# Performance work log

Hardware: AMD Instinct MI355X
Metric: run time of the kernel (lower is better)

Reference implementation:

```python
import jax, jax.numpy as jnp
import numpy as np

B, S, D, H = 2, 2048, 1024, 16
DH = D // H
NEG = -1000000.0


def setup_inputs() -> dict:
    key = jax.random.key(0)
    k1, k2, k3, k4, k5, k6 = jax.random.split(key, 6)
    query = jax.random.normal(k1, (B, S, D), dtype=jnp.float32)
    key_t = jax.random.normal(k2, (B, S, D), dtype=jnp.float32)
    value = jax.random.normal(k3, (B, S, D), dtype=jnp.float32)
    # causal boolean mask, broadcast to [B*H, S, S] as the torch module expects
    causal = jnp.tril(jnp.ones((S, S), dtype=bool))
    attn_mask = jnp.broadcast_to(causal, (B * H, S, S))
    WQ = jax.random.normal(k4, (D, D), dtype=jnp.float32) * 0.02
    WK = jax.random.normal(k5, (D, D), dtype=jnp.float32) * 0.02
    WV = jax.random.normal(k6, (D, D), dtype=jnp.float32) * 0.02
    return {"query": query, "key": key_t, "value": value,
            "attn_mask": attn_mask, "WQ": WQ, "WK": WK, "WV": WV}


def reference(query, key, value, attn_mask, WQ, WK, WV):
    b, s, d = query.shape
    h = attn_mask.shape[0] // b
    dh = d // h
    # Linear projections (bias=False) then torch's split(dim=2)+concat(dim=0)
    # == reshape to [b,s,h,dh] and move head axis to the front: [h,b,s,dh]
    q = (query @ WQ).reshape(b, s, h, dh).transpose(2, 0, 1, 3)
    k = (key @ WK).reshape(b, s, h, dh).transpose(2, 0, 1, 3)
    v = (value @ WV).reshape(b, s, h, dh).transpose(2, 0, 1, 3)
    mask = attn_mask.reshape(h, b, s, s)
    add_mask = jnp.where(mask, jnp.float32(0.0), jnp.float32(NEG))
    # NOTE: original adds the mask BEFORE dividing by sqrt(dh) (baddbmm then /=)
    scores = (jnp.einsum('hbqd,hbkd->hbqk', q, k) + add_mask) / jnp.float32(dh ** 0.5)
    p = jax.nn.softmax(scores, axis=-1)
    p = p * mask.astype(p.dtype)  # mask applied a second time post-softmax
    out = jnp.einsum('hbqk,hbkd->hbqd', p, v)  # [h,b,s,dh]
    # concat heads back on the feature dim: [b,s,d]
    return out.transpose(1, 2, 0, 3).reshape(b, s, d)
```

## Files before the change

kernel.cpp:

```cpp
#include <hip/hip_runtime.h>
#include <hip/hip_bf16.h>

#define B_  2
#define S_  2048
#define D_  1024
#define H_  16
#define DH_ 64
#define BH_ (B_ * H_)
#define M_  (B_ * S_)

typedef __bf16 bf16x8 __attribute__((ext_vector_type(8)));
typedef __bf16 bf16x4 __attribute__((ext_vector_type(4)));
typedef float  f32x4  __attribute__((ext_vector_type(4)));

__device__ __forceinline__ __bf16 to_bf16(float f) {
  union { float f; unsigned u; } un; un.f = f;
  unsigned r = un.u + 0x7FFFu + ((un.u >> 16) & 1u);
  union { unsigned short s; __bf16 b; } o;
  o.s = (unsigned short)(r >> 16);
  return o.b;
}

__device__ __forceinline__ void async_load16(const __bf16* g, __bf16* l) {
  __builtin_amdgcn_global_load_lds(
      (const __attribute__((address_space(1))) void*)g,
      (__attribute__((address_space(3))) void*)l, 16, 0, 0);
}

__global__ __launch_bounds__(256) void convert_x_kernel(
    const float* __restrict__ q_in, const float* __restrict__ k_in,
    const float* __restrict__ v_in, __bf16* __restrict__ Xb) {
  const float* src = blockIdx.z == 0 ? q_in : (blockIdx.z == 1 ? k_in : v_in);
  __bf16* dst = Xb + (size_t)blockIdx.z * M_ * D_;
  const size_t i = ((size_t)blockIdx.x * 256 + threadIdx.x) * 4;
  const float4 f = *(const float4*)(src + i);
  bf16x4 o;
  o[0] = to_bf16(f.x); o[1] = to_bf16(f.y); o[2] = to_bf16(f.z); o[3] = to_bf16(f.w);
  *(bf16x4*)(dst + i) = o;
}

__global__ void transpose_w_kernel(const float* __restrict__ Wq,
                                   const float* __restrict__ Wk,
                                   const float* __restrict__ Wv,
                                   __bf16* __restrict__ WT) {
  __shared__ float tile[32][33];
  const float* src = blockIdx.z == 0 ? Wq : (blockIdx.z == 1 ? Wk : Wv);
  __bf16* dst = WT + (size_t)blockIdx.z * D_ * D_;
  const int tx = threadIdx.x, ty = threadIdx.y;
  const int j  = blockIdx.x * 32 + tx;
  const int k0 = blockIdx.y * 32;
#pragma unroll
  for (int i = 0; i < 32; i += 8)
    tile[ty + i][tx] = src[(size_t)(k0 + ty + i) * D_ + j];
  __syncthreads();
  const int jr = blockIdx.x * 32;
  const int kc = k0 + tx;
#pragma unroll
  for (int i = 0; i < 32; i += 8)
    dst[(size_t)(jr + ty + i) * D_ + kc] = to_bf16(tile[tx][ty + i]);
}

__global__ __launch_bounds__(256) void proj_kernel(
    const __bf16* __restrict__ Xb, const __bf16* __restrict__ WT,
    __bf16* __restrict__ Qo, __bf16* __restrict__ Ko, __bf16* __restrict__ VTo) {
  const int lane = threadIdx.x & 63;
  const int wave = threadIdx.x >> 6;
  const int lr   = lane & 15;
  const int quad = lane >> 4;
  const int wr   = wave >> 1;
  const int wc   = wave & 1;
  const int which = blockIdx.z;
  const __bf16* X  = Xb + (size_t)which * M_ * D_;
  const __bf16* Wt = WT + (size_t)which * D_ * D_;
  const int m0 = blockIdx.y * 128;
  const int n0 = blockIdx.x * 128;

  __shared__ __align__(16) __bf16 As[128 * 32];
  __shared__ __align__(16) __bf16 Bs[128 * 32];

  f32x4 acc[4][4];
#pragma unroll
  for (int a = 0; a < 4; ++a)
#pragma unroll
    for (int b = 0; b < 4; ++b)
      acc[a][b] = f32x4{0.f, 0.f, 0.f, 0.f};

  const int srow  = (lane >> 2);
  const int schnk = (lane & 3) * 8;

  for (int kt = 0; kt < D_ / 32; ++kt) {
    const int k0 = kt * 32;
#pragma unroll
    for (int r16 = 0; r16 < 2; ++r16) {
      const int row = wave * 32 + r16 * 16 + srow;
      async_load16(X  + (size_t)(m0 + row) * D_ + k0 + schnk,
                   As + (size_t)(wave * 32 + r16 * 16) * 32);
      async_load16(Wt + (size_t)(n0 + row) * D_ + k0 + schnk,
                   Bs + (size_t)(wave * 32 + r16 * 16) * 32);
    }
    __syncthreads();

    bf16x8 af[4], bf[4];
#pragma unroll
    for (int mi = 0; mi < 4; ++mi)
      af[mi] = *(const bf16x8*)(As + (size_t)(wr * 64 + mi * 16 + lr) * 32 + quad * 8);
#pragma unroll
    for (int ni = 0; ni < 4; ++ni)
      bf[ni] = *(const bf16x8*)(Bs + (size_t)(wc * 64 + ni * 16 + lr) * 32 + quad * 8);
#pragma unroll
    for (int mi = 0; mi < 4; ++mi)
#pragma unroll
      for (int ni = 0; ni < 4; ++ni)
        acc[mi][ni] = __builtin_amdgcn_mfma_f32_16x16x32_bf16(af[mi], bf[ni], acc[mi][ni], 0, 0, 0);
    __syncthreads();
  }

#pragma unroll
  for (int mi = 0; mi < 4; ++mi)
#pragma unroll
    for (int ni = 0; ni < 4; ++ni)
#pragma unroll
      for (int r = 0; r < 4; ++r) {
        const int gm = m0 + wr * 64 + mi * 16 + quad * 4 + r;
        const int gn = n0 + wc * 64 + ni * 16 + lr;
        const int b  = gm >> 11;
        const int s  = gm & (S_ - 1);
        const int h  = gn >> 6;
        const int dh = gn & (DH_ - 1);
        const int bh = b * H_ + h;
        const __bf16 bv = to_bf16(acc[mi][ni][r]);
        if (which == 0)      Qo [((size_t)bh * S_ + s)  * DH_ + dh] = bv;
        else if (which == 1) Ko [((size_t)bh * S_ + s)  * DH_ + dh] = bv;
        else                 VTo[((size_t)bh * DH_ + dh) * S_ + s]  = bv;
      }
}

__global__ __launch_bounds__(64) void attn_kernel(
    const __bf16* __restrict__ Q, const __bf16* __restrict__ K,
    const __bf16* __restrict__ VT, float* __restrict__ out) {
  const int lane = threadIdx.x;
  const int lr   = lane & 15;
  const int quad = lane >> 4;
  const int qt = (gridDim.x - 1) - blockIdx.x;
  const int bh = blockIdx.y;
  const int q0 = qt * 32;
  const __bf16* Qb = Q  + (size_t)bh * S_ * DH_;
  const __bf16* Kb = K  + (size_t)bh * S_ * DH_;
  const __bf16* Vb = VT + (size_t)bh * DH_ * S_;

  bf16x8 qa[2][2];
#pragma unroll
  for (int rt = 0; rt < 2; ++rt)
#pragma unroll
    for (int hh = 0; hh < 2; ++hh)
      qa[rt][hh] = *(const bf16x8*)(Qb + (size_t)(q0 + rt * 16 + lr) * DH_ + hh * 32 + quad * 8);

  f32x4 o[2][4];
#pragma unroll
  for (int rt = 0; rt < 2; ++rt)
#pragma unroll
    for (int dt = 0; dt < 4; ++dt) o[rt][dt] = f32x4{0.f, 0.f, 0.f, 0.f};
  float lsum[2][4];
#pragma unroll
  for (int rt = 0; rt < 2; ++rt)
#pragma unroll
    for (int r = 0; r < 4; ++r) lsum[rt][r] = 0.f;

  __shared__ __align__(16) __bf16 Pb[32][72];

  const int ntiles = qt / 2 + 1;
  for (int kt = 0; kt < ntiles; ++kt) {
    const int k0 = kt * 64;
    const bool full = (k0 + 63) <= q0;
    const f32x4 zero = f32x4{0.f, 0.f, 0.f, 0.f};
    f32x4 s[2][4];
#pragma unroll
    for (int c = 0; c < 4; ++c) {
      bf16x8 kb0 = *(const bf16x8*)(Kb + (size_t)(k0 + c * 16 + lr) * DH_ + quad * 8);
      bf16x8 kb1 = *(const bf16x8*)(Kb + (size_t)(k0 + c * 16 + lr) * DH_ + 32 + quad * 8);
#pragma unroll
      for (int rt = 0; rt < 2; ++rt) {
        s[rt][c] = __builtin_amdgcn_mfma_f32_16x16x32_bf16(qa[rt][0], kb0, zero,     0, 0, 0);
        s[rt][c] = __builtin_amdgcn_mfma_f32_16x16x32_bf16(qa[rt][1], kb1, s[rt][c], 0, 0, 0);
      }
    }
#pragma unroll
    for (int rt = 0; rt < 2; ++rt)
#pragma unroll
      for (int c = 0; c < 4; ++c)
#pragma unroll
        for (int r = 0; r < 4; ++r) {
          const int row = q0 + rt * 16 + quad * 4 + r;
          const int col = k0 + c * 16 + lr;
          float p = __expf(s[rt][c][r] * 0.125f);
          if (!full && col > row) p = 0.f;
          lsum[rt][r] += p;
          Pb[rt * 16 + quad * 4 + r][c * 16 + lr] = to_bf16(p);
        }
    __syncthreads();
    bf16x8 vb[4][2];
#pragma unroll
    for (int dt = 0; dt < 4; ++dt) {
      vb[dt][0] = *(const bf16x8*)(Vb + (size_t)(dt * 16 + lr) * S_ + k0 + quad * 8);
      vb[dt][1] = *(const bf16x8*)(Vb + (size_t)(dt * 16 + lr) * S_ + k0 + 32 + quad * 8);
    }
#pragma unroll
    for (int rt = 0; rt < 2; ++rt) {
      const bf16x8 pa0 = *(const bf16x8*)(&Pb[rt * 16 + lr][quad * 8]);
      const bf16x8 pa1 = *(const bf16x8*)(&Pb[rt * 16 + lr][32 + quad * 8]);
#pragma unroll
      for (int dt = 0; dt < 4; ++dt) {
        o[rt][dt] = __builtin_amdgcn_mfma_f32_16x16x32_bf16(pa0, vb[dt][0], o[rt][dt], 0, 0, 0);
        o[rt][dt] = __builtin_amdgcn_mfma_f32_16x16x32_bf16(pa1, vb[dt][1], o[rt][dt], 0, 0, 0);
      }
    }
    __syncthreads();
  }

  const int b = bh / H_;
  const int h = bh % H_;
#pragma unroll
  for (int rt = 0; rt < 2; ++rt)
#pragma unroll
    for (int r = 0; r < 4; ++r) {
      float l = lsum[rt][r];
      l += __shfl_xor(l, 1);
      l += __shfl_xor(l, 2);
      l += __shfl_xor(l, 4);
      l += __shfl_xor(l, 8);
      const float inv = 1.0f / l;
      const int row = q0 + rt * 16 + quad * 4 + r;
      float* orow = out + ((size_t)(b * S_ + row)) * D_ + h * DH_;
#pragma unroll
      for (int dt = 0; dt < 4; ++dt)
        orow[dt * 16 + lr] = o[rt][dt][r] * inv;
    }
}

extern "C" void kernel_launch(void* const* d_in, const int* in_sizes, int n_in,
                              void* d_out, int out_size, void* d_ws, size_t ws_size,
                              hipStream_t stream) {
  const float* q_in = (const float*)d_in[0];
  const float* k_in = (const float*)d_in[1];
  const float* v_in = (const float*)d_in[2];
  const float* wq   = (const float*)d_in[4];
  const float* wk   = (const float*)d_in[5];
  const float* wv   = (const float*)d_in[6];

  __bf16* ws  = (__bf16*)d_ws;
  __bf16* Xb  = ws;
  __bf16* WT  = Xb + (size_t)3 * M_ * D_;
  __bf16* Qo  = WT + (size_t)3 * D_ * D_;
  __bf16* Ko  = Qo + (size_t)BH_ * S_ * DH_;
  __bf16* VTo = Ko + (size_t)BH_ * S_ * DH_;
  float* outp = (float*)d_out;

  convert_x_kernel<<<dim3(M_ * D_ / 1024, 1, 3), 256, 0, stream>>>(q_in, k_in, v_in, Xb);
  transpose_w_kernel<<<dim3(D_ / 32, D_ / 32, 3), dim3(32, 8), 0, stream>>>(wq, wk, wv, WT);
  proj_kernel<<<dim3(D_ / 128, M_ / 128, 3), 256, 0, stream>>>(Xb, WT, Qo, Ko, VTo);
  attn_kernel<<<dim3(S_ / 32, BH_), 64, 0, stream>>>(Qo, Ko, VTo, outp);
}
```

Baseline: 803.9 us.

## Transpose MFMA operand order to vectorize bf16 stores in projection and attention

Measured after the change: 774.9 us. 3.6% less time.

```diff
diff --git a/kernel.cpp b/kernel.cpp
--- a/kernel.cpp
+++ b/kernel.cpp
@@ -19,6 +19,18 @@
   union { unsigned short s; __bf16 b; } o;
   o.s = (unsigned short)(r >> 16);
   return o.b;
+}
+
+__device__ __forceinline__ uint2 pack4_rne(f32x4 v) {
+  union { __bf16 b[4]; uint2 u; } o;
+#pragma unroll
+  for (int i = 0; i < 4; ++i) o.b[i] = to_bf16(v[i]);
+  return o.u;
+}
+
+__device__ __forceinline__ unsigned pack2_fast(float lo, float hi) {
+  return ((__float_as_uint(hi) + 0x8000u) & 0xFFFF0000u) |
+         ((__float_as_uint(lo) + 0x8000u) >> 16);
 }
 
 __device__ __forceinline__ void async_load16(const __bf16* g, __bf16* l) {
@@ -100,39 +112,59 @@
     }
     __syncthreads();
 
-    bf16x8 af[4], bf[4];
+    bf16x8 af[4], bfr[4];
 #pragma unroll
     for (int mi = 0; mi < 4; ++mi)
       af[mi] = *(const bf16x8*)(As + (size_t)(wr * 64 + mi * 16 + lr) * 32 + quad * 8);
 #pragma unroll
     for (int ni = 0; ni < 4; ++ni)
-      bf[ni] = *(const bf16x8*)(Bs + (size_t)(wc * 64 + ni * 16 + lr) * 32 + quad * 8);
-#pragma unroll
-    for (int mi = 0; mi < 4; ++mi)
-#pragma unroll
-      for (int ni = 0; ni < 4; ++ni)
-        acc[mi][ni] = __builtin_amdgcn_mfma_f32_16x16x32_bf16(af[mi], bf[ni], acc[mi][ni], 0, 0, 0);
+      bfr[ni] = *(const bf16x8*)(Bs + (size_t)(wc * 64 + ni * 16 + lr) * 32 + quad * 8);
+    if (which != 2) {
+#pragma unroll
+      for (int mi = 0; mi < 4; ++mi)
+#pragma unroll
+        for (int ni = 0; ni < 4; ++ni)
+          acc[mi][ni] = __builtin_amdgcn_mfma_f32_16x16x32_bf16(bfr[ni], af[mi], acc[mi][ni], 0, 0, 0);
+    } else {
+#pragma unroll
+      for (int mi = 0; mi < 4; ++mi)
+#pragma unroll
+        for (int ni = 0; ni < 4; ++ni)
+          acc[mi][ni] = __builtin_amdgcn_mfma_f32_16x16x32_bf16(af[mi], bfr[ni], acc[mi][ni], 0, 0, 0);
+    }
     __syncthreads();
   }
 
-#pragma unroll
-  for (int mi = 0; mi < 4; ++mi)
-#pragma unroll
-    for (int ni = 0; ni < 4; ++ni)
-#pragma unroll
-      for (int r = 0; r < 4; ++r) {
-        const int gm = m0 + wr * 64 + mi * 16 + quad * 4 + r;
-        const int gn = n0 + wc * 64 + ni * 16 + lr;
-        const int b  = gm >> 11;
-        const int s  = gm & (S_ - 1);
-        const int h  = gn >> 6;
-        const int dh = gn & (DH_ - 1);
-        const int bh = b * H_ + h;
-        const __bf16 bv = to_bf16(acc[mi][ni][r]);
-        if (which == 0)      Qo [((size_t)bh * S_ + s)  * DH_ + dh] = bv;
-        else if (which == 1) Ko [((size_t)bh * S_ + s)  * DH_ + dh] = bv;
-        else                 VTo[((size_t)bh * DH_ + dh) * S_ + s]  = bv;
-      }
+  if (which != 2) {
+    __bf16* dst = which == 0 ? Qo : Ko;
+#pragma unroll
+    for (int mi = 0; mi < 4; ++mi)
+#pragma unroll
+      for (int ni = 0; ni < 4; ++ni) {
+        const int gm  = m0 + wr * 64 + mi * 16 + lr;
+        const int gn0 = n0 + wc * 64 + ni * 16 + quad * 4;
+        const int b   = gm >> 11;
+        const int s   = gm & (S_ - 1);
+        const int h   = gn0 >> 6;
+        const int dh0 = gn0 & (DH_ - 1);
+        const int bh  = b * H_ + h;
+        *(uint2*)(dst + ((size_t)bh * S_ + s) * DH_ + dh0) = pack4_rne(acc[mi][ni]);
+      }
+  } else {
+#pragma unroll
+    for (int mi = 0; mi < 4; ++mi)
+#pragma unroll
+      for (int ni = 0; ni < 4; ++ni) {
+        const int gm0 = m0 + wr * 64 + mi * 16 + quad * 4;
+        const int gn  = n0 + wc * 64 + ni * 16 + lr;
+        const int b   = gm0 >> 11;
+        const int s0  = gm0 & (S_ - 1);
+        const int h   = gn >> 6;
+        const int dh  = gn & (DH_ - 1);
+        const int bh  = b * H_ + h;
+        *(uint2*)(VTo + ((size_t)bh * DH_ + dh) * S_ + s0) = pack4_rne(acc[mi][ni]);
+      }
+  }
 }
 
 __global__ __launch_bounds__(64) void attn_kernel(
@@ -147,6 +179,7 @@
   const __bf16* Qb = Q  + (size_t)bh * S_ * DH_;
   const __bf16* Kb = K  + (size_t)bh * S_ * DH_;
   const __bf16* Vb = VT + (size_t)bh * DH_ * S_;
+  const float CEXP = 0.18033688011112042f;
 
   bf16x8 qa[2][2];
 #pragma unroll
@@ -160,50 +193,57 @@
   for (int rt = 0; rt < 2; ++rt)
 #pragma unroll
     for (int dt = 0; dt < 4; ++dt) o[rt][dt] = f32x4{0.f, 0.f, 0.f, 0.f};
-  float lsum[2][4];
-#pragma unroll
-  for (int rt = 0; rt < 2; ++rt)
-#pragma unroll
-    for (int r = 0; r < 4; ++r) lsum[rt][r] = 0.f;
-
-  __shared__ __align__(16) __bf16 Pb[32][72];
+  float lsum[2] = {0.f, 0.f};
+
+  __shared__ __align__(16) __bf16 Pb[32][68];
 
   const int ntiles = qt / 2 + 1;
   for (int kt = 0; kt < ntiles; ++kt) {
     const int k0 = kt * 64;
     const bool full = (k0 + 63) <= q0;
     const f32x4 zero = f32x4{0.f, 0.f, 0.f, 0.f};
-    f32x4 s[2][4];
+
+    bf16x8 kb[4][2], vb[4][2];
 #pragma unroll
     for (int c = 0; c < 4; ++c) {
-      bf16x8 kb0 = *(const bf16x8*)(Kb + (size_t)(k0 + c * 16 + lr) * DH_ + quad * 8);
-      bf16x8 kb1 = *(const bf16x8*)(Kb + (size_t)(k0 + c * 16 + lr) * DH_ + 32 + quad * 8);
-#pragma unroll
-      for (int rt = 0; rt < 2; ++rt) {
-        s[rt][c] = __builtin_amdgcn_mfma_f32_16x16x32_bf16(qa[rt][0], kb0, zero,     0, 0, 0);
-        s[rt][c] = __builtin_amdgcn_mfma_f32_16x16x32_bf16(qa[rt][1], kb1, s[rt][c], 0, 0, 0);
-      }
-    }
-#pragma unroll
-    for (int rt = 0; rt < 2; ++rt)
-#pragma unroll
-      for (int c = 0; c < 4; ++c)
-#pragma unroll
-        for (int r = 0; r < 4; ++r) {
-          const int row = q0 + rt * 16 + quad * 4 + r;
-          const int col = k0 + c * 16 + lr;
-          float p = __expf(s[rt][c][r] * 0.125f);
-          if (!full && col > row) p = 0.f;
-          lsum[rt][r] += p;
-          Pb[rt * 16 + quad * 4 + r][c * 16 + lr] = to_bf16(p);
-        }
-    __syncthreads();
-    bf16x8 vb[4][2];
+      kb[c][0] = *(const bf16x8*)(Kb + (size_t)(k0 + c * 16 + lr) * DH_ + quad * 8);
+      kb[c][1] = *(const bf16x8*)(Kb + (size_t)(k0 + c * 16 + lr) * DH_ + 32 + quad * 8);
+    }
 #pragma unroll
     for (int dt = 0; dt < 4; ++dt) {
       vb[dt][0] = *(const bf16x8*)(Vb + (size_t)(dt * 16 + lr) * S_ + k0 + quad * 8);
       vb[dt][1] = *(const bf16x8*)(Vb + (size_t)(dt * 16 + lr) * S_ + k0 + 32 + quad * 8);
     }
+
+    f32x4 st[2][4];
+#pragma unroll
+    for (int c = 0; c < 4; ++c)
+#pragma unroll
+      for (int rt = 0; rt < 2; ++rt) {
+        st[rt][c] = __builtin_amdgcn_mfma_f32_16x16x32_bf16(kb[c][0], qa[rt][0], zero,      0, 0, 0);
+        st[rt][c] = __builtin_amdgcn_mfma_f32_16x16x32_bf16(kb[c][1], qa[rt][1], st[rt][c], 0, 0, 0);
+      }
+
+#pragma unroll
+    for (int rt = 0; rt < 2; ++rt) {
+      const int qrow = q0 + rt * 16 + lr;
+#pragma unroll
+      for (int c = 0; c < 4; ++c) {
+        float p[4];
+#pragma unroll
+        for (int r = 0; r < 4; ++r) {
+          const int key = k0 + c * 16 + quad * 4 + r;
+          float pv = exp2f(st[rt][c][r] * CEXP);
+          if (!full && key > qrow) pv = 0.f;
+          p[r] = pv;
+          lsum[rt] += pv;
+        }
+        uint2 w; w.x = pack2_fast(p[0], p[1]); w.y = pack2_fast(p[2], p[3]);
+        *(uint2*)(&Pb[rt * 16 + lr][c * 16 + quad * 4]) = w;
+      }
+    }
+    __syncthreads();
+
 #pragma unroll
     for (int rt = 0; rt < 2; ++rt) {
       const bf16x8 pa0 = *(const bf16x8*)(&Pb[rt * 16 + lr][quad * 8]);
@@ -220,21 +260,21 @@
   const int b = bh / H_;
   const int h = bh % H_;
 #pragma unroll
-  for (int rt = 0; rt < 2; ++rt)
+  for (int rt = 0; rt < 2; ++rt) {
+    float l = lsum[rt];
+    l += __shfl_xor(l, 16);
+    l += __shfl_xor(l, 32);
+    const float inv = 1.0f / l;
 #pragma unroll
     for (int r = 0; r < 4; ++r) {
-      float l = lsum[rt][r];
-      l += __shfl_xor(l, 1);
-      l += __shfl_xor(l, 2);
-      l += __shfl_xor(l, 4);
-      l += __shfl_xor(l, 8);
-      const float inv = 1.0f / l;
+      const float invr = __shfl(inv, quad * 4 + r);
       const int row = q0 + rt * 16 + quad * 4 + r;
       float* orow = out + ((size_t)(b * S_ + row)) * D_ + h * DH_;
 #pragma unroll
       for (int dt = 0; dt < 4; ++dt)
-        orow[dt * 16 + lr] = o[rt][dt][r] * inv;
-    }
+        orow[dt * 16 + lr] = o[rt][dt][r] * invr;
+    }
+  }
 }
 
 extern "C" void kernel_launch(void* const* d_in, const int* in_sizes, int n_in,
```
